# Performance work log

Measured on AMD Instinct MI355X. Metric: run time of the kernel, lower is better.

Reference implementation:

```python
import jax, jax.numpy as jnp
import numpy as np

B, H, L, D = 2, 16, 2048, 64
EPS = 1e-6  # guard for all-zero causal rows after ReLU feature map


def setup_inputs() -> dict:
    key = jax.random.key(0)
    k1, k2, k3, k4, k5 = jax.random.split(key, 5)
    return {
        "query_states": jax.random.normal(k1, (B, H, L, D), dtype=jnp.float32),
        "key_states": jax.random.normal(k2, (B, H, L, D), dtype=jnp.float32),
        "value_states": jax.random.normal(k3, (B, H, L, D), dtype=jnp.float32),
        # LinearFeatureMap params: nn.Parameter(torch.rand(H, D, D)) -> uniform[0,1)
        "fm_query": jax.random.uniform(k4, (H, D, D), dtype=jnp.float32),
        "fm_key": jax.random.uniform(k5, (H, D, D), dtype=jnp.float32),
    }


def _feature_map(states, w):
    # states: [B,H,L,D]; w: [H,D,E]. Matches einsum('blhd,hde->blhe') after transposes.
    return jax.nn.relu(jnp.einsum('bhld,hde->bhle', states, w))


def reference(query_states, key_states, value_states, fm_query, fm_key):
    q = _feature_map(query_states, fm_query)   # [B,H,L,E]
    k = _feature_map(key_states, fm_key)       # [B,H,L,E]
    # quadratic (non-softmax) causal attention
    a = jnp.einsum('bhme,bhne->bhmn', q, k)    # [B,H,L,L]
    causal = jnp.tril(jnp.ones((L, L), dtype=bool))
    a = jnp.where(causal, a, 0.0)
    a = a / (jnp.sum(a, axis=-1, keepdims=True) + EPS)
    return jnp.einsum('bhmn,bhnd->bhmd', a, value_states)
```

## Files before the change

kernel.cpp:

```cpp
#include <hip/hip_runtime.h>
#include <hip/hip_bf16.h>

#define BH_  32
#define H_   16
#define L_   2048
#define D_   64
#define NC_  32
#define STR  72

typedef _Float16 half8 __attribute__((ext_vector_type(8)));
typedef _Float16 half4 __attribute__((ext_vector_type(4)));
typedef _Float16 half2v __attribute__((ext_vector_type(2)));
typedef float    floatx4 __attribute__((ext_vector_type(4)));

#define MFMA(a, b, c) __builtin_amdgcn_mfma_f32_16x16x32_f16((a), (b), (c), 0, 0, 0)

__device__ __forceinline__ half8 ldfrag(const _Float16* p, int row0, int k0) {
    const int lane = threadIdx.x & 63;
    const _Float16* q = p + (row0 + (lane & 15)) * STR + k0 + ((lane >> 4) << 3);
    return *(const half8*)q;
}

__global__ __launch_bounds__(256)
void k0_weights(const float* __restrict__ Wq, const float* __restrict__ Wk,
                _Float16* __restrict__ WqTh, _Float16* __restrict__ WqTl,
                _Float16* __restrict__ WkT) {
    __shared__ float sQ[64 * 65];
    __shared__ float sK[64 * 65];
    const int h = blockIdx.x, tid = threadIdx.x;
    const float* Wqg = Wq + (size_t)h * 4096;
    const float* Wkg = Wk + (size_t)h * 4096;
    for (int i = 0; i < 16; ++i) {
        int flat = i * 256 + tid;
        int d = flat >> 6, e = flat & 63;
        sQ[e * 65 + d] = Wqg[flat];
        sK[e * 65 + d] = Wkg[flat];
    }
    __syncthreads();
    for (int i = 0; i < 4; ++i) {
        int flat = i * 1024 + tid * 4;
        int e = flat >> 6, d0 = flat & 63;
        half4 qh, ql, kh;
        #pragma unroll
        for (int j = 0; j < 4; ++j) {
            float qv = sQ[e * 65 + d0 + j];
            _Float16 hi = (_Float16)qv;
            qh[j] = hi; ql[j] = (_Float16)(qv - (float)hi);
            kh[j] = (_Float16)sK[e * 65 + d0 + j];
        }
        *(half4*)(WqTh + (size_t)h * 4096 + flat) = qh;
        *(half4*)(WqTl + (size_t)h * 4096 + flat) = ql;
        *(half4*)(WkT  + (size_t)h * 4096 + flat) = kh;
    }
}

__global__ __launch_bounds__(256, 2)
void ka_chunksum(const float* __restrict__ K, const float* __restrict__ V,
                 const _Float16* __restrict__ WkT,
                 _Float16* __restrict__ Ss, float* __restrict__ zc,
                 _Float16* __restrict__ kf16, _Float16* __restrict__ VT16) {
    __shared__ __align__(16) _Float16 sK  [64 * STR];
    __shared__ __align__(16) _Float16 sWkT[64 * STR];
    __shared__ __align__(16) _Float16 sVT [64 * STR];
    __shared__ __align__(16) _Float16 sKfT[64 * STR];

    const int c = blockIdx.x, bh = blockIdx.y, h = bh & (H_ - 1);
    const int tid = threadIdx.x, lane = tid & 63, w = tid >> 6;
    const int quad = lane >> 4, cl = lane & 15;

    const float* Kg = K + ((size_t)bh * L_ + c * 64) * D_;
    const float* Vg = V + ((size_t)bh * L_ + c * 64) * D_;
    const size_t cb = (size_t)bh * NC_ + c;

    for (int i = 0; i < 4; ++i) {
        int flat = i * 1024 + tid * 4;
        int r = flat >> 6, e0 = flat & 63;
        float4 kv = *(const float4*)(Kg + flat);
        half4 kh = { (_Float16)kv.x, (_Float16)kv.y, (_Float16)kv.z, (_Float16)kv.w };
        *(half4*)(sK + r * STR + e0) = kh;
        float4 vv = *(const float4*)(Vg + flat);
        sVT[(e0 + 0) * STR + r] = (_Float16)vv.x;
        sVT[(e0 + 1) * STR + r] = (_Float16)vv.y;
        sVT[(e0 + 2) * STR + r] = (_Float16)vv.z;
        sVT[(e0 + 3) * STR + r] = (_Float16)vv.w;
    }
    for (int i = 0; i < 2; ++i) {
        int flat = i * 2048 + tid * 8;
        int e = flat >> 6, d0 = flat & 63;
        *(half8*)(sWkT + e * STR + d0) = *(const half8*)(WkT + (size_t)h * 4096 + flat);
    }
    __syncthreads();

    half8 ak0 = ldfrag(sK, w * 16, 0), ak1 = ldfrag(sK, w * 16, 32);
    for (int et = 0; et < 4; ++et) {
        floatx4 acc = {0.f, 0.f, 0.f, 0.f};
        acc = MFMA(ak0, ldfrag(sWkT, et * 16, 0),  acc);
        acc = MFMA(ak1, ldfrag(sWkT, et * 16, 32), acc);
        #pragma unroll
        for (int r = 0; r < 4; ++r) {
            float v = acc[r] > 0.f ? acc[r] : 0.f;
            _Float16 hv = (_Float16)v;
            int n = w * 16 + quad * 4 + r, f = et * 16 + cl;
            sKfT[f * STR + n] = hv;
            sK  [n * STR + f] = hv;
        }
    }
    __syncthreads();

    for (int i = 0; i < 2; ++i) {
        int flat = i * 2048 + tid * 8;
        int rr = flat >> 6, c0 = flat & 63;
        *(half8*)(kf16 + cb * 4096 + flat) = *(const half8*)(sK  + rr * STR + c0);
        *(half8*)(VT16 + cb * 4096 + flat) = *(const half8*)(sVT + rr * STR + c0);
    }
    if (tid < 64) {
        float s = 0.f;
        #pragma unroll
        for (int j = 0; j < 8; ++j) {
            half8 hv = *(const half8*)(sKfT + tid * STR + j * 8);
            #pragma unroll
            for (int t = 0; t < 8; ++t) s += (float)hv[t];
        }
        zc[cb * 64 + tid] = s;
    }

    _Float16* So = Ss + cb * 4096;
    half8 av0 = ldfrag(sVT, w * 16, 0), av1 = ldfrag(sVT, w * 16, 32);
    for (int et = 0; et < 4; ++et) {
        floatx4 acc = {0.f, 0.f, 0.f, 0.f};
        acc = MFMA(av0, ldfrag(sKfT, et * 16, 0),  acc);
        acc = MFMA(av1, ldfrag(sKfT, et * 16, 32), acc);
        #pragma unroll
        for (int r = 0; r < 4; ++r)
            So[(w * 16 + quad * 4 + r) * 64 + et * 16 + cl] = (_Float16)acc[r];
    }
}

__global__ __launch_bounds__(64)
void kp_prefix(_Float16* __restrict__ Ss, float* __restrict__ zc) {
    const int bid = blockIdx.x, t = threadIdx.x;
    if (bid < BH_ * 32) {
        const int bh = bid >> 5, dq = bid & 31;
        uint32_t* S32 = (uint32_t*)Ss;
        size_t base = (size_t)bh * NC_ * 2048 + dq * 64 + t;
        float r0 = 0.f, r1 = 0.f;
        #pragma unroll
        for (int c = 0; c < NC_; ++c) {
            uint32_t u = S32[base + (size_t)c * 2048];
            half2v hv = *(half2v*)&u;
            float v0 = (float)hv[0], v1 = (float)hv[1];
            half2v o; o[0] = (_Float16)r0; o[1] = (_Float16)r1;
            S32[base + (size_t)c * 2048] = *(uint32_t*)&o;
            r0 += v0; r1 += v1;
        }
    } else {
        const int bh = bid - BH_ * 32;
        size_t base = (size_t)bh * NC_ * 64 + t;
        float run = 0.f;
        #pragma unroll
        for (int c = 0; c < NC_; ++c) {
            float v = zc[base + c * 64];
            zc[base + c * 64] = run;
            run += v;
        }
    }
}

__global__ __launch_bounds__(256, 3)
void kb_attn(const float* __restrict__ Q, const _Float16* __restrict__ WqTh,
             const _Float16* __restrict__ WqTl, const _Float16* __restrict__ kf16,
             const _Float16* __restrict__ VT16, const _Float16* __restrict__ Ss,
             const float* __restrict__ zs, float* __restrict__ Out) {
    __shared__ __align__(16) _Float16 sQh[64 * STR];
    __shared__ __align__(16) _Float16 sQl[64 * STR];
    __shared__ __align__(16) _Float16 sWh[64 * STR];
    __shared__ __align__(16) _Float16 sWl[64 * STR];
    __shared__ __align__(16) _Float16 sKf[64 * STR];
    __shared__ float sZ[64];

    const int c = blockIdx.x, bh = blockIdx.y, h = bh & (H_ - 1);
    const int tid = threadIdx.x, lane = tid & 63, w = tid >> 6;
    const int quad = lane >> 4, cl = lane & 15;

    const float* Qg = Q + ((size_t)bh * L_ + c * 64) * D_;
    const size_t cb = (size_t)bh * NC_ + c;
    const _Float16* Sgp = Ss   + cb * 4096;
    const _Float16* Vgp = VT16 + cb * 4096;

    for (int i = 0; i < 4; ++i) {
        int flat = i * 1024 + tid * 4;
        int r = flat >> 6, e0 = flat & 63;
        float4 qv = *(const float4*)(Qg + flat);
        half4 qh, ql;
        #pragma unroll
        for (int j = 0; j < 4; ++j) {
            float x = (&qv.x)[j];
            _Float16 hi = (_Float16)x;
            qh[j] = hi; ql[j] = (_Float16)(x - (float)hi);
        }
        *(half4*)(sQh + r * STR + e0) = qh;
        *(half4*)(sQl + r * STR + e0) = ql;
    }
    for (int i = 0; i < 2; ++i) {
        int flat = i * 2048 + tid * 8;
        int rr = flat >> 6, c0 = flat & 63;
        *(half8*)(sWh + rr * STR + c0) = *(const half8*)(WqTh + (size_t)h * 4096 + flat);
        *(half8*)(sWl + rr * STR + c0) = *(const half8*)(WqTl + (size_t)h * 4096 + flat);
        *(half8*)(sKf + rr * STR + c0) = *(const half8*)(kf16 + cb * 4096 + flat);
    }
    if (tid < 64) sZ[tid] = zs[cb * 64 + tid];
    __syncthreads();

    half8 aqh0 = ldfrag(sQh, w * 16, 0), aqh1 = ldfrag(sQh, w * 16, 32);
    half8 aql0 = ldfrag(sQl, w * 16, 0), aql1 = ldfrag(sQl, w * 16, 32);
    float dq[4] = {0.f, 0.f, 0.f, 0.f};
    for (int et = 0; et < 4; ++et) {
        half8 bh0 = ldfrag(sWh, et * 16, 0), bh1 = ldfrag(sWh, et * 16, 32);
        half8 bl0 = ldfrag(sWl, et * 16, 0), bl1 = ldfrag(sWl, et * 16, 32);
        floatx4 acc = {0.f, 0.f, 0.f, 0.f};
        acc = MFMA(aqh0, bh0, acc);
        acc = MFMA(aqh1, bh1, acc);
        acc = MFMA(aqh0, bl0, acc);
        acc = MFMA(aqh1, bl1, acc);
        acc = MFMA(aql0, bh0, acc);
        acc = MFMA(aql1, bh1, acc);
        float zv = sZ[et * 16 + cl];
        #pragma unroll
        for (int r = 0; r < 4; ++r) {
            float v = acc[r] > 0.f ? acc[r] : 0.f;
            dq[r] += v * zv;
            sQh[(w * 16 + quad * 4 + r) * STR + et * 16 + cl] = (_Float16)v;
        }
    }
    #pragma unroll
    for (int r = 0; r < 4; ++r) {
        dq[r] += __shfl_xor(dq[r], 1);
        dq[r] += __shfl_xor(dq[r], 2);
        dq[r] += __shfl_xor(dq[r], 4);
        dq[r] += __shfl_xor(dq[r], 8);
    }

    half8 qh0 = ldfrag(sQh, w * 16, 0), qh1 = ldfrag(sQh, w * 16, 32);
    _Float16* P = sQl;
    float rs[4] = {0.f, 0.f, 0.f, 0.f};
    float inv[4];
    for (int nt = 0; nt <= w; ++nt) {
        floatx4 acc = {0.f, 0.f, 0.f, 0.f};
        acc = MFMA(qh0, ldfrag(sKf, nt * 16, 0),  acc);
        acc = MFMA(qh1, ldfrag(sKf, nt * 16, 32), acc);
        #pragma unroll
        for (int r = 0; r < 4; ++r) {
            float v = acc[r];
            if (nt == w && cl > quad * 4 + r) v = 0.f;
            rs[r] += v;
            P[(w * 16 + quad * 4 + r) * STR + nt * 16 + cl] = (_Float16)v;
        }
    }
    for (int nt = w + 1; nt < 4; ++nt) {
        #pragma unroll
        for (int r = 0; r < 4; ++r)
            P[(w * 16 + quad * 4 + r) * STR + nt * 16 + cl] = (_Float16)0.f;
    }
    #pragma unroll
    for (int r = 0; r < 4; ++r) {
        float s = rs[r];
        s += __shfl_xor(s, 1);
        s += __shfl_xor(s, 2);
        s += __shfl_xor(s, 4);
        s += __shfl_xor(s, 8);
        inv[r] = 1.f / (s + dq[r] + 1e-6f);
    }

    half8 p0 = ldfrag(P, w * 16, 0), p1 = ldfrag(P, w * 16, 32);
    float* Og = Out + ((size_t)bh * L_ + c * 64) * D_;
    for (int et = 0; et < 4; ++et) {
        const _Float16* srow = Sgp + (et * 16 + cl) * 64 + quad * 8;
        const _Float16* vrow = Vgp + (et * 16 + cl) * 64 + quad * 8;
        half8 s0 = *(const half8*)(srow);
        half8 s1 = *(const half8*)(srow + 32);
        half8 v0 = *(const half8*)(vrow);
        half8 v1 = *(const half8*)(vrow + 32);
        floatx4 acc = {0.f, 0.f, 0.f, 0.f};
        acc = MFMA(qh0, s0, acc);
        acc = MFMA(qh1, s1, acc);
        acc = MFMA(p0,  v0, acc);
        acc = MFMA(p1,  v1, acc);
        #pragma unroll
        for (int r = 0; r < 4; ++r)
            Og[(w * 16 + quad * 4 + r) * 64 + et * 16 + cl] = acc[r] * inv[r];
    }
}

extern "C" void kernel_launch(void* const* d_in, const int* in_sizes, int n_in,
                              void* d_out, int out_size, void* d_ws, size_t ws_size,
                              hipStream_t stream) {
    const float* Q  = (const float*)d_in[0];
    const float* K  = (const float*)d_in[1];
    const float* V  = (const float*)d_in[2];
    const float* Wq = (const float*)d_in[3];
    const float* Wk = (const float*)d_in[4];
    float* Out = (float*)d_out;

    _Float16* Ss   = (_Float16*)d_ws;
    float*    zc   = (float*)(Ss + (size_t)BH_ * NC_ * 4096);
    _Float16* kf16 = (_Float16*)(zc + (size_t)BH_ * NC_ * 64);
    _Float16* VT16 = kf16 + (size_t)BH_ * NC_ * 4096;
    _Float16* WqTh = VT16 + (size_t)BH_ * NC_ * 4096;
    _Float16* WqTl = WqTh + (size_t)H_ * 4096;
    _Float16* WkT  = WqTl + (size_t)H_ * 4096;

    dim3 grid(NC_, BH_);
    hipLaunchKernelGGL(k0_weights, dim3(H_), dim3(256), 0, stream, Wq, Wk, WqTh, WqTl, WkT);
    hipLaunchKernelGGL(ka_chunksum, grid, dim3(256), 0, stream, K, V, WkT, Ss, zc, kf16, VT16);
    hipLaunchKernelGGL(kp_prefix, dim3(BH_ * 32 + BH_), dim3(64), 0, stream, Ss, zc);
    hipLaunchKernelGGL(kb_attn, grid, dim3(256), 0, stream, Q, WqTh, WqTl, kf16, VT16, Ss, zc, Out);
}
```

Before: 120.6 us.

## Fuse weight prep and prefix scan into chunk kernel via last-block atomic

Removes the separate weight-transpose kernel: each chunk block and attention block now loads the fp32 weights directly, transposes them and converts them to fp16 (hi/lo split for Wq) in shared memory. The separate prefix-scan kernel is also removed. The last block per (b,h) to finish is detected with an atomic counter, and that block performs the exclusive prefix over chunk states and normalizers. This cuts the launch count from four kernels to two plus a memset. In exchange, the weight conversion is redone in every block, and the serial scan is done by a single block per head instead of 32 parallel blocks.

After: 292.4 us. +142.5%, slower.

```diff
diff --git a/kernel.cpp b/kernel.cpp
--- a/kernel.cpp
+++ b/kernel.cpp
@@ -21,48 +21,17 @@
     return *(const half8*)q;
 }
 
-__global__ __launch_bounds__(256)
-void k0_weights(const float* __restrict__ Wq, const float* __restrict__ Wk,
-                _Float16* __restrict__ WqTh, _Float16* __restrict__ WqTl,
-                _Float16* __restrict__ WkT) {
-    __shared__ float sQ[64 * 65];
-    __shared__ float sK[64 * 65];
-    const int h = blockIdx.x, tid = threadIdx.x;
-    const float* Wqg = Wq + (size_t)h * 4096;
-    const float* Wkg = Wk + (size_t)h * 4096;
-    for (int i = 0; i < 16; ++i) {
-        int flat = i * 256 + tid;
-        int d = flat >> 6, e = flat & 63;
-        sQ[e * 65 + d] = Wqg[flat];
-        sK[e * 65 + d] = Wkg[flat];
-    }
-    __syncthreads();
-    for (int i = 0; i < 4; ++i) {
-        int flat = i * 1024 + tid * 4;
-        int e = flat >> 6, d0 = flat & 63;
-        half4 qh, ql, kh;
-        #pragma unroll
-        for (int j = 0; j < 4; ++j) {
-            float qv = sQ[e * 65 + d0 + j];
-            _Float16 hi = (_Float16)qv;
-            qh[j] = hi; ql[j] = (_Float16)(qv - (float)hi);
-            kh[j] = (_Float16)sK[e * 65 + d0 + j];
-        }
-        *(half4*)(WqTh + (size_t)h * 4096 + flat) = qh;
-        *(half4*)(WqTl + (size_t)h * 4096 + flat) = ql;
-        *(half4*)(WkT  + (size_t)h * 4096 + flat) = kh;
-    }
-}
-
 __global__ __launch_bounds__(256, 2)
-void ka_chunksum(const float* __restrict__ K, const float* __restrict__ V,
-                 const _Float16* __restrict__ WkT,
-                 _Float16* __restrict__ Ss, float* __restrict__ zc,
-                 _Float16* __restrict__ kf16, _Float16* __restrict__ VT16) {
+void ka_fused(const float* __restrict__ K, const float* __restrict__ V,
+              const float* __restrict__ Wk,
+              _Float16* __restrict__ Ss, float* __restrict__ zc,
+              _Float16* __restrict__ kf16, _Float16* __restrict__ VT16,
+              int* __restrict__ cnt) {
     __shared__ __align__(16) _Float16 sK  [64 * STR];
     __shared__ __align__(16) _Float16 sWkT[64 * STR];
     __shared__ __align__(16) _Float16 sVT [64 * STR];
     __shared__ __align__(16) _Float16 sKfT[64 * STR];
+    __shared__ int sLast;
 
     const int c = blockIdx.x, bh = blockIdx.y, h = bh & (H_ - 1);
     const int tid = threadIdx.x, lane = tid & 63, w = tid >> 6;
@@ -70,6 +39,7 @@
 
     const float* Kg = K + ((size_t)bh * L_ + c * 64) * D_;
     const float* Vg = V + ((size_t)bh * L_ + c * 64) * D_;
+    const float* Wkg = Wk + (size_t)h * 4096;
     const size_t cb = (size_t)bh * NC_ + c;
 
     for (int i = 0; i < 4; ++i) {
@@ -83,11 +53,11 @@
         sVT[(e0 + 1) * STR + r] = (_Float16)vv.y;
         sVT[(e0 + 2) * STR + r] = (_Float16)vv.z;
         sVT[(e0 + 3) * STR + r] = (_Float16)vv.w;
-    }
-    for (int i = 0; i < 2; ++i) {
-        int flat = i * 2048 + tid * 8;
-        int e = flat >> 6, d0 = flat & 63;
-        *(half8*)(sWkT + e * STR + d0) = *(const half8*)(WkT + (size_t)h * 4096 + flat);
+        float4 wv = *(const float4*)(Wkg + flat);
+        sWkT[(e0 + 0) * STR + r] = (_Float16)wv.x;
+        sWkT[(e0 + 1) * STR + r] = (_Float16)wv.y;
+        sWkT[(e0 + 2) * STR + r] = (_Float16)wv.z;
+        sWkT[(e0 + 3) * STR + r] = (_Float16)wv.w;
     }
     __syncthreads();
 
@@ -134,43 +104,53 @@
         for (int r = 0; r < 4; ++r)
             So[(w * 16 + quad * 4 + r) * 64 + et * 16 + cl] = (_Float16)acc[r];
     }
+
+    __threadfence();
+    __syncthreads();
+    if (tid == 0) sLast = (atomicAdd(&cnt[bh], 1) == NC_ - 1) ? 1 : 0;
+    __syncthreads();
+    if (!sLast) return;
+    __threadfence();
+
+    uint32_t* S32 = (uint32_t*)(Ss + (size_t)bh * NC_ * 4096);
+    float run[16];
+    #pragma unroll
+    for (int j = 0; j < 16; ++j) run[j] = 0.f;
+    for (int cc = 0; cc < NC_; ++cc) {
+        uint32_t* p = S32 + cc * 2048 + tid * 8;
+        uint4 a = *(uint4*)p, b = *(uint4*)(p + 4);
+        uint32_t in[8] = {a.x, a.y, a.z, a.w, b.x, b.y, b.z, b.w};
+        uint32_t out[8];
+        #pragma unroll
+        for (int j = 0; j < 8; ++j) {
+            half2v hv = *(half2v*)&in[j];
+            half2v o; o[0] = (_Float16)run[2*j]; o[1] = (_Float16)run[2*j+1];
+            out[j] = *(uint32_t*)&o;
+            run[2*j]   += (float)hv[0];
+            run[2*j+1] += (float)hv[1];
+        }
+        uint4 oa = {out[0], out[1], out[2], out[3]};
+        uint4 ob = {out[4], out[5], out[6], out[7]};
+        *(uint4*)p = oa;
+        *(uint4*)(p + 4) = ob;
+    }
+    if (tid < 64) {
+        float* zb = zc + (size_t)bh * NC_ * 64;
+        float r = 0.f;
+        #pragma unroll
+        for (int cc = 0; cc < NC_; ++cc) {
+            float v = zb[cc * 64 + tid];
+            zb[cc * 64 + tid] = r;
+            r += v;
+        }
+    }
 }
 
-__global__ __launch_bounds__(64)
-void kp_prefix(_Float16* __restrict__ Ss, float* __restrict__ zc) {
-    const int bid = blockIdx.x, t = threadIdx.x;
-    if (bid < BH_ * 32) {
-        const int bh = bid >> 5, dq = bid & 31;
-        uint32_t* S32 = (uint32_t*)Ss;
-        size_t base = (size_t)bh * NC_ * 2048 + dq * 64 + t;
-        float r0 = 0.f, r1 = 0.f;
-        #pragma unroll
-        for (int c = 0; c < NC_; ++c) {
-            uint32_t u = S32[base + (size_t)c * 2048];
-            half2v hv = *(half2v*)&u;
-            float v0 = (float)hv[0], v1 = (float)hv[1];
-            half2v o; o[0] = (_Float16)r0; o[1] = (_Float16)r1;
-            S32[base + (size_t)c * 2048] = *(uint32_t*)&o;
-            r0 += v0; r1 += v1;
-        }
-    } else {
-        const int bh = bid - BH_ * 32;
-        size_t base = (size_t)bh * NC_ * 64 + t;
-        float run = 0.f;
-        #pragma unroll
-        for (int c = 0; c < NC_; ++c) {
-            float v = zc[base + c * 64];
-            zc[base + c * 64] = run;
-            run += v;
-        }
-    }
-}
-
 __global__ __launch_bounds__(256, 3)
-void kb_attn(const float* __restrict__ Q, const _Float16* __restrict__ WqTh,
-             const _Float16* __restrict__ WqTl, const _Float16* __restrict__ kf16,
-             const _Float16* __restrict__ VT16, const _Float16* __restrict__ Ss,
-             const float* __restrict__ zs, float* __restrict__ Out) {
+void kb_attn(const float* __restrict__ Q, const float* __restrict__ Wq,
+             const _Float16* __restrict__ kf16, const _Float16* __restrict__ VT16,
+             const _Float16* __restrict__ Ss, const float* __restrict__ zs,
+             float* __restrict__ Out) {
     __shared__ __align__(16) _Float16 sQh[64 * STR];
     __shared__ __align__(16) _Float16 sQl[64 * STR];
     __shared__ __align__(16) _Float16 sWh[64 * STR];
@@ -183,6 +163,7 @@
     const int quad = lane >> 4, cl = lane & 15;
 
     const float* Qg = Q + ((size_t)bh * L_ + c * 64) * D_;
+    const float* Wqg = Wq + (size_t)h * 4096;
     const size_t cb = (size_t)bh * NC_ + c;
     const _Float16* Sgp = Ss   + cb * 4096;
     const _Float16* Vgp = VT16 + cb * 4096;
@@ -200,12 +181,18 @@
         }
         *(half4*)(sQh + r * STR + e0) = qh;
         *(half4*)(sQl + r * STR + e0) = ql;
+        float4 wv = *(const float4*)(Wqg + flat);
+        #pragma unroll
+        for (int j = 0; j < 4; ++j) {
+            float x = (&wv.x)[j];
+            _Float16 hi = (_Float16)x;
+            sWh[(e0 + j) * STR + r] = hi;
+            sWl[(e0 + j) * STR + r] = (_Float16)(x - (float)hi);
+        }
     }
     for (int i = 0; i < 2; ++i) {
         int flat = i * 2048 + tid * 8;
         int rr = flat >> 6, c0 = flat & 63;
-        *(half8*)(sWh + rr * STR + c0) = *(const half8*)(WqTh + (size_t)h * 4096 + flat);
-        *(half8*)(sWl + rr * STR + c0) = *(const half8*)(WqTl + (size_t)h * 4096 + flat);
         *(half8*)(sKf + rr * STR + c0) = *(const half8*)(kf16 + cb * 4096 + flat);
     }
     if (tid < 64) sZ[tid] = zs[cb * 64 + tid];
@@ -305,13 +292,10 @@
     float*    zc   = (float*)(Ss + (size_t)BH_ * NC_ * 4096);
     _Float16* kf16 = (_Float16*)(zc + (size_t)BH_ * NC_ * 64);
     _Float16* VT16 = kf16 + (size_t)BH_ * NC_ * 4096;
-    _Float16* WqTh = VT16 + (size_t)BH_ * NC_ * 4096;
-    _Float16* WqTl = WqTh + (size_t)H_ * 4096;
-    _Float16* WkT  = WqTl + (size_t)H_ * 4096;
-
+    int*      cnt  = (int*)(VT16 + (size_t)BH_ * NC_ * 4096);
+
+    hipMemsetAsync(cnt, 0, BH_ * sizeof(int), stream);
     dim3 grid(NC_, BH_);
-    hipLaunchKernelGGL(k0_weights, dim3(H_), dim3(256), 0, stream, Wq, Wk, WqTh, WqTl, WkT);
-    hipLaunchKernelGGL(ka_chunksum, grid, dim3(256), 0, stream, K, V, WkT, Ss, zc, kf16, VT16);
-    hipLaunchKernelGGL(kp_prefix, dim3(BH_ * 32 + BH_), dim3(64), 0, stream, Ss, zc);
-    hipLaunchKernelGGL(kb_attn, grid, dim3(256), 0, stream, Q, WqTh, WqTl, kf16, VT16, Ss, zc, Out);
+    hipLaunchKernelGGL(ka_fused, grid, dim3(256), 0, stream, K, V, Wk, Ss, zc, kf16, VT16, cnt);
+    hipLaunchKernelGGL(kb_attn, grid, dim3(256), 0, stream, Q, Wq, kf16, VT16, Ss, zc, Out);
 }
```
